# Kernel tuning notes

Hardware: AMD Instinct MI355X
Metric: run time of the kernel (lower is better)

Reference implementation:

```python
import jax, jax.numpy as jnp
import numpy as np
from jax import lax

B, N, NPOINT, NSAMPLE = 16, 8192, 1024, 32
RADIUS = 0.2
EPS = 1e-5


def setup_inputs() -> dict:
    key = jax.random.key(0)
    ks = jax.random.split(key, 6)
    return {
        "xyz": jax.random.uniform(ks[0], (B, N, 3), dtype=jnp.float32),
        "points": jax.random.normal(ks[1], (B, N, 64), dtype=jnp.float32),
        "w1": jax.random.normal(ks[2], (64, 67), dtype=jnp.float32) * 0.1,
        "b1": jnp.zeros((64,), jnp.float32),
        "g1": jnp.ones((64,), jnp.float32),
        "be1": jnp.zeros((64,), jnp.float32),
        "w2": jax.random.normal(ks[3], (64, 64), dtype=jnp.float32) * 0.1,
        "b2": jnp.zeros((64,), jnp.float32),
        "g2": jnp.ones((64,), jnp.float32),
        "be2": jnp.zeros((64,), jnp.float32),
        "w3": jax.random.normal(ks[4], (128, 64), dtype=jnp.float32) * 0.1,
        "b3": jnp.zeros((128,), jnp.float32),
        "g3": jnp.ones((128,), jnp.float32),
        "be3": jnp.zeros((128,), jnp.float32),
    }


def farthest_point_sample(xyz, npoint):
    # Sequential FPS; deterministic start at index 0 (torch uses a random start).
    b, n, _ = xyz.shape
    batch_ix = jnp.arange(b)

    def step(carry, _):
        distance, farthest = carry
        centroid = xyz[batch_ix, farthest]              # [B,3]
        dist = jnp.sum((xyz - centroid[:, None, :]) ** 2, -1)  # [B,N]
        distance = jnp.minimum(distance, dist)
        return (distance, jnp.argmax(distance, -1).astype(jnp.int32)), farthest

    init = (jnp.full((b, n), 1e10, jnp.float32), jnp.zeros((b,), jnp.int32))
    _, idxs = lax.scan(step, init, None, length=npoint)
    return idxs.T                                        # [B,npoint]


def gather_points(points, idx):
    # points [B,N,C], idx [B,...] -> [B,...,C]
    return jax.vmap(lambda p, i: p[i])(points, idx)


def query_ball_point(radius, nsample, xyz, new_xyz):
    b, n, _ = xyz.shape
    sqrd = jnp.sum((new_xyz[:, :, None, :] - xyz[:, None, :, :]) ** 2, -1)  # [B,S,N]
    gidx = jnp.where(sqrd > radius ** 2, n, jnp.arange(n, dtype=jnp.int32)[None, None, :])
    gidx = jnp.sort(gidx, axis=-1)[:, :, :nsample]       # [B,S,K]
    first = gidx[:, :, :1]
    return jnp.where(gidx == n, first, gidx)


def conv_bn_relu(x, w, b, g, be):
    # x [B,C,S,K]; 1x1 conv == channel matmul, then train-mode BN over (B,S,K).
    y = jnp.einsum("bcsk,oc->bosk", x, w) + b[None, :, None, None]
    mean = jnp.mean(y, axis=(0, 2, 3), keepdims=True)
    var = jnp.mean((y - mean) ** 2, axis=(0, 2, 3), keepdims=True)
    yhat = (y - mean) * lax.rsqrt(var + EPS)
    return jax.nn.relu(yhat * g[None, :, None, None] + be[None, :, None, None])


def reference(xyz, points, w1, b1, g1, be1, w2, b2, g2, be2, w3, b3, g3, be3):
    fps_idx = farthest_point_sample(xyz, NPOINT)          # [B,S]
    new_xyz = gather_points(xyz, fps_idx)                 # [B,S,3]
    idx = query_ball_point(RADIUS, NSAMPLE, xyz, new_xyz) # [B,S,K]
    grouped_xyz = gather_points(xyz, idx)                 # [B,S,K,3]
    grouped_xyz_norm = grouped_xyz - new_xyz[:, :, None, :]
    grouped_points = gather_points(points, idx)           # [B,S,K,64]
    new_points = jnp.concatenate([grouped_xyz_norm, grouped_points], axis=-1)
    x = jnp.transpose(new_points, (0, 3, 1, 2))           # [B,67,S,K]
    x = conv_bn_relu(x, w1, b1, g1, be1)
    x = conv_bn_relu(x, w2, b2, g2, be2)
    x = conv_bn_relu(x, w3, b3, g3, be3)
    new_points_out = jnp.max(x, axis=-1)                  # [B,128,S]
    return new_xyz, new_points_out
```

## Files before the change

kernel.cpp:

```cpp
#include <hip/hip_runtime.h>
#include <hip/hip_bf16.h>

typedef unsigned short u16;
typedef unsigned long long u64;
typedef __attribute__((ext_vector_type(8))) short short8;
typedef __attribute__((ext_vector_type(4))) float f32x4;

#define NN 8192
#define SSAMP 1024
#define KK 32
#define NT_F 524288.0f
#define EPSV 1e-5f

__device__ __forceinline__ u64 umax64(u64 a, u64 b) { return a > b ? a : b; }

template <int C>
__device__ __forceinline__ void dppstep(unsigned& hi, unsigned& lo) {
  unsigned h2 = (unsigned)__builtin_amdgcn_update_dpp(0, (int)hi, C, 0xF, 0xF, true);
  unsigned l2 = (unsigned)__builtin_amdgcn_update_dpp(0, (int)lo, C, 0xF, 0xF, true);
  u64 a = ((u64)hi << 32) | lo;
  u64 b = ((u64)h2 << 32) | l2;
  bool g = b > a;
  hi = g ? h2 : hi;
  lo = g ? l2 : lo;
}

__device__ __forceinline__ u64 wave_max_key(u64 key) {
  unsigned hi = (unsigned)(key >> 32), lo = (unsigned)key;
  dppstep<0x111>(hi, lo);
  dppstep<0x112>(hi, lo);
  dppstep<0x114>(hi, lo);
  dppstep<0x118>(hi, lo);
  dppstep<0x142>(hi, lo);
  dppstep<0x143>(hi, lo);
  return ((u64)hi << 32) | lo;
}

__device__ __forceinline__ int morton3(int ix, int iy, int iz) {
  int m = (((ix >> 0) & 1) << 2) | (((iy >> 0) & 1) << 1) | (((iz >> 0) & 1) << 0);
  m |= (((ix >> 1) & 1) << 5) | (((iy >> 1) & 1) << 4) | (((iz >> 1) & 1) << 3);
  m |= (((ix >> 2) & 1) << 8) | (((iy >> 2) & 1) << 7) | (((iz >> 2) & 1) << 6);
  return m;
}

__global__ __launch_bounds__(1024, 1) void fps_bucket_kernel(const float* __restrict__ xyz,
                                                             float* __restrict__ newxyz) {
  extern __shared__ float dynls[];
  float* sx = dynls;
  float* sy = dynls + NN;
  float* sz = dynls + 2 * NN;
  int* sI = (int*)(dynls + 3 * NN);
  __shared__ int cnt[512], off[512];
  __shared__ u64 candS[3];
  __shared__ int pos0_sh;

  const int b = blockIdx.x, t = threadIdx.x;
  const float* base = xyz + (size_t)b * NN * 3;

  float px[8], py[8], pz[8];
  int pc[8];
  if (t < 512) cnt[t] = 0;
  if (t == 0) { candS[0] = 0; candS[1] = 0; candS[2] = 0; }
  __syncthreads();
#pragma unroll
  for (int j = 0; j < 8; j++) {
    int p = j * 1024 + t;
    px[j] = base[p * 3 + 0];
    py[j] = base[p * 3 + 1];
    pz[j] = base[p * 3 + 2];
    int ix = min(7, (int)(px[j] * 8.0f));
    int iy = min(7, (int)(py[j] * 8.0f));
    int iz = min(7, (int)(pz[j] * 8.0f));
    pc[j] = morton3(ix, iy, iz);
    atomicAdd(&cnt[pc[j]], 1);
  }
  __syncthreads();
  int myc = (t < 512) ? cnt[t] : 0;
  for (int st = 1; st < 512; st <<= 1) {
    int v = 0;
    if (t < 512) { v = cnt[t]; if (t >= st) v += cnt[t - st]; }
    __syncthreads();
    if (t < 512) cnt[t] = v;
    __syncthreads();
  }
  if (t < 512) off[t] = cnt[t] - myc;
  __syncthreads();
#pragma unroll
  for (int j = 0; j < 8; j++) {
    int pos = atomicAdd(&off[pc[j]], 1);
    sx[pos] = px[j]; sy[pos] = py[j]; sz[pos] = pz[j];
    int orig = j * 1024 + t;
    sI[pos] = orig;
    if (orig == 0) pos0_sh = pos;
  }
  __syncthreads();
  float X[8], Y[8], Z[8], D[8];
  unsigned L26[8];
  float lox = 1e30f, loy = 1e30f, loz = 1e30f;
  float hix = -1e30f, hiy = -1e30f, hiz = -1e30f;
#pragma unroll
  for (int j = 0; j < 8; j++) {
    int p = t * 8 + j;
    float x = sx[p], y = sy[p], z = sz[p];
    X[j] = x; Y[j] = y; Z[j] = z; D[j] = 1e10f;
    int orig = sI[p];
    L26[j] = ((unsigned)(8191 - orig) << 13) | (unsigned)p;
    lox = fminf(lox, x); hix = fmaxf(hix, x);
    loy = fminf(loy, y); hiy = fmaxf(hiy, y);
    loz = fminf(loz, z); hiz = fmaxf(hiz, z);
  }
  int cur = pos0_sh;
  u64 ckey = 0;
  float cbd = 1e30f;
  u64 wkeyS = 0;
  int s = 0;

  for (int it = 0; it < SSAMP; it++) {
    const int sn = (s == 2) ? 0 : s + 1;
    float cx = sx[cur], cy = sy[cur], cz = sz[cur];
    if (t == 0) {
      float* o = newxyz + ((size_t)b * SSAMP + it) * 3;
      o[0] = cx; o[1] = cy; o[2] = cz;
    }
    float ddx = fmaxf(fmaxf(lox - cx, cx - hix), 0.f);
    float ddy = fmaxf(fmaxf(loy - cy, cy - hiy), 0.f);
    float ddz = fmaxf(fmaxf(loz - cz, cz - hiz), 0.f);
    float lb2 = fmaf(ddx, ddx, fmaf(ddy, ddy, ddz * ddz));
    bool upd = lb2 <= fmaf(cbd, 1.0001f, 1e-12f);
    if (__ballot(upd)) {
      if (upd) {
        u64 k = 0;
        float bd = -1.0f;
#pragma unroll
        for (int j = 0; j < 8; j++) {
          float dx = __fsub_rn(X[j], cx);
          float dy = __fsub_rn(Y[j], cy);
          float dz = __fsub_rn(Z[j], cz);
          float d = __fadd_rn(__fadd_rn(__fmul_rn(dx, dx), __fmul_rn(dy, dy)), __fmul_rn(dz, dz));
          float dm = fminf(D[j], d);
          D[j] = dm;
          bd = fmaxf(bd, dm);
          u64 kj = ((u64)__float_as_uint(dm) << 26) | (u64)L26[j];
          k = umax64(k, kj);
        }
        ckey = k;
        cbd = bd;
      }
      wkeyS = wave_max_key(ckey);
    }
    if ((t & 63) == 63) atomicMax(&candS[s], wkeyS);
    if (t == 0) candS[sn] = 0;
    __syncthreads();
    cur = (int)(candS[s] & 0x1FFFull);
    s = sn;
  }
}

__global__ __launch_bounds__(512, 1) void fps_fallback_kernel(const float* __restrict__ xyz,
                                                              float* __restrict__ newxyz) {
  const int b = blockIdx.x, t = threadIdx.x;
  const float* base = xyz + (size_t)b * NN * 3;
  __shared__ u64 cand[2][8];
  float X[16], Y[16], Z[16], D[16];
#pragma unroll
  for (int j = 0; j < 16; j++) {
    int p = j * 512 + t;
    X[j] = base[p * 3 + 0];
    Y[j] = base[p * 3 + 1];
    Z[j] = base[p * 3 + 2];
    D[j] = 1e10f;
  }
  __syncthreads();
  int cur = 0;
  const int w = t >> 6;
  for (int it = 0; it < SSAMP; it++) {
    float cx = base[cur * 3 + 0];
    float cy = base[cur * 3 + 1];
    float cz = base[cur * 3 + 2];
    if (t == 0) {
      float* o = newxyz + ((size_t)b * SSAMP + it) * 3;
      o[0] = cx; o[1] = cy; o[2] = cz;
    }
    float bestd = -1.0f;
    int bj = 0;
#pragma unroll
    for (int j = 0; j < 16; j++) {
      float dx = __fsub_rn(X[j], cx);
      float dy = __fsub_rn(Y[j], cy);
      float dz = __fsub_rn(Z[j], cz);
      float d = __fadd_rn(__fadd_rn(__fmul_rn(dx, dx), __fmul_rn(dy, dy)), __fmul_rn(dz, dz));
      float dm = fminf(D[j], d);
      D[j] = dm;
      bool g = dm > bestd;
      bestd = g ? dm : bestd;
      bj = g ? j : bj;
    }
    u64 key = ((u64)__float_as_uint(bestd) << 32) |
              (u64)(unsigned)~(unsigned)(bj * 512 + t);
    key = wave_max_key(key);
    const int s = it & 1;
    if ((t & 63) == 63) cand[s][w] = key;
    __syncthreads();
    u64 c0 = cand[s][0], c1 = cand[s][1], c2 = cand[s][2], c3 = cand[s][3];
    u64 c4 = cand[s][4], c5 = cand[s][5], c6 = cand[s][6], c7 = cand[s][7];
    u64 a0 = umax64(c0, c1), a1 = umax64(c2, c3), a2 = umax64(c4, c5), a3 = umax64(c6, c7);
    u64 best = umax64(umax64(a0, a1), umax64(a2, a3));
    cur = (int)(~(unsigned)(best & 0xFFFFFFFFull));
  }
}

__global__ __launch_bounds__(256) void ballq_kernel(const float* __restrict__ xyz,
                                                    const float* __restrict__ newxyz,
                                                    int* __restrict__ ballidx) {
  const int wid = blockIdx.x * 4 + (threadIdx.x >> 6);
  const int lane = threadIdx.x & 63;
  const int b = wid >> 10;
  const float* base = xyz + (size_t)b * NN * 3;
  const float cx = newxyz[wid * 3 + 0];
  const float cy = newxyz[wid * 3 + 1];
  const float cz = newxyz[wid * 3 + 2];
  int* op = ballidx + (size_t)wid * KK;
  int cnt = 0, first = -1;
  for (int p0 = 0; p0 < NN; p0 += 64) {
    const int p = p0 + lane;
    float dx = __fsub_rn(cx, base[p * 3 + 0]);
    float dy = __fsub_rn(cy, base[p * 3 + 1]);
    float dz = __fsub_rn(cz, base[p * 3 + 2]);
    float d = __fadd_rn(__fadd_rn(__fmul_rn(dx, dx), __fmul_rn(dy, dy)), __fmul_rn(dz, dz));
    bool hit = d <= 0.04f;
    u64 m = __ballot(hit);
    if (m) {
      if (first < 0) first = p0 + __ffsll((long long)m) - 1;
      int rank = __popcll(m & ((1ull << lane) - 1ull));
      int slot = cnt + rank;
      if (hit && slot < KK) op[slot] = p;
      cnt += __popcll(m);
      if (cnt >= KK) break;
    }
  }
  if (cnt < KK && lane >= cnt && lane < KK) op[lane] = first;
}

__device__ __forceinline__ void stage_W(const float* __restrict__ w, float* Ws, int K, int O, int t) {
  for (int i2 = t; i2 < K * O; i2 += 256) {
    int c = i2 / O, o = i2 % O;
    Ws[i2] = w[o * K + c];
  }
}

__global__ __launch_bounds__(256) void gemm1_kernel(const float* __restrict__ xyz,
                                                    const float* __restrict__ pts,
                                                    const float* __restrict__ w1,
                                                    const float* __restrict__ b1,
                                                    const float* __restrict__ newxyz,
                                                    const int* __restrict__ ballidx,
                                                    u16* __restrict__ Y1,
                                                    float* __restrict__ bkt) {
  __shared__ __align__(16) float As[67 * 64];
  __shared__ __align__(16) float Ws[67 * 64];
  __shared__ int sidx[64];
  __shared__ float snx[6];
  const int t = threadIdx.x, blk = blockIdx.x;
  const int pbase = blk * 64;
  const int g0 = pbase >> 5;
  const int b = g0 >> 10;
  if (t < 64) sidx[t] = ballidx[pbase + t];
  if (t < 6) snx[t] = newxyz[(size_t)g0 * 3 + t];
  stage_W(w1, Ws, 67, 64, t);
  __syncthreads();
  {
    int r = t >> 2, q = t & 3;
    const float4* prow = (const float4*)(pts + ((size_t)b * NN + sidx[r]) * 64);
#pragma unroll
    for (int l = 0; l < 4; l++) {
      float4 v = prow[q * 4 + l];
      int c = 3 + q * 16 + l * 4;
      As[(c + 0) * 64 + r] = v.x;
      As[(c + 1) * 64 + r] = v.y;
      As[(c + 2) * 64 + r] = v.z;
      As[(c + 3) * 64 + r] = v.w;
    }
  }
  if (t < 64) {
    const float* xp = xyz + ((size_t)b * NN + sidx[t]) * 3;
    int g = t >> 5;
    As[0 * 64 + t] = xp[0] - snx[g * 3 + 0];
    As[1 * 64 + t] = xp[1] - snx[g * 3 + 1];
    As[2 * 64 + t] = xp[2] - snx[g * 3 + 2];
  }
  __syncthreads();
  const int i = t & 15, j = t >> 4;
  float acc[4][4];
#pragma unroll
  for (int a = 0; a < 4; a++)
#pragma unroll
    for (int c2 = 0; c2 < 4; c2++) acc[a][c2] = 0.f;
#pragma unroll 4
  for (int c = 0; c < 67; c++) {
    float4 a4 = *(const float4*)&As[c * 64 + i * 4];
    float4 w4 = *(const float4*)&Ws[c * 64 + j * 4];
    float av[4] = {a4.x, a4.y, a4.z, a4.w};
    float wv[4] = {w4.x, w4.y, w4.z, w4.w};
#pragma unroll
    for (int ii = 0; ii < 4; ii++)
#pragma unroll
      for (int jj = 0; jj < 4; jj++) acc[ii][jj] = fmaf(av[ii], wv[jj], acc[ii][jj]);
  }
  float bl[4];
#pragma unroll
  for (int jj = 0; jj < 4; jj++) bl[jj] = b1[j * 4 + jj];
#pragma unroll
  for (int ii = 0; ii < 4; ii++) {
    union { ushort4 u4; __hip_bfloat16 h[4]; } pk;
#pragma unroll
    for (int jj = 0; jj < 4; jj++) {
      float y = acc[ii][jj] + bl[jj];
      acc[ii][jj] = y;
      pk.h[jj] = __float2bfloat16(y);
    }
    *(ushort4*)&Y1[((size_t)(pbase + i * 4 + ii)) * 64 + j * 4] = pk.u4;
  }
  float sums[4], sqs[4];
#pragma unroll
  for (int jj = 0; jj < 4; jj++) {
    float s = 0.f, q2 = 0.f;
#pragma unroll
    for (int ii = 0; ii < 4; ii++) { float v = acc[ii][jj]; s += v; q2 += v * v; }
    sums[jj] = s; sqs[jj] = q2;
  }
#pragma unroll
  for (int off = 1; off < 16; off <<= 1) {
#pragma unroll
    for (int jj = 0; jj < 4; jj++) {
      sums[jj] += __shfl_xor(sums[jj], off);
      sqs[jj] += __shfl_xor(sqs[jj], off);
    }
  }
  if ((t & 15) == 0) {
    float* bb = bkt + (size_t)(blk & 63) * 512;
#pragma unroll
    for (int jj = 0; jj < 4; jj++) {
      atomicAdd(&bb[j * 4 + jj], sums[jj]);
      atomicAdd(&bb[64 + j * 4 + jj], sqs[jj]);
    }
  }
}

__global__ __launch_bounds__(256) void collapse_kernel(const float* __restrict__ bkt,
                                                       float* __restrict__ dst) {
  int e = blockIdx.x * 256 + threadIdx.x;
  float s = 0.f;
#pragma unroll 8
  for (int u = 0; u < 64; u++) s += bkt[u * 512 + e];
  dst[e] = s;
}

__device__ __forceinline__ short8 bn_pack8(const u16 h[8], const float* sS, const float* sT, int c0) {
  short8 r;
#pragma unroll
  for (int x = 0; x < 8; x++) {
    float f = __bfloat162float(*(const __hip_bfloat16*)&h[x]);
    f = fmaxf(fmaf(f, sS[c0 + x], sT[c0 + x]), 0.f);
    __hip_bfloat16 hb = __float2bfloat16(f);
    r[x] = *(const short*)&hb;
  }
  return r;
}

__device__ __forceinline__ short8 w_pack8(const float v[8]) {
  short8 r;
#pragma unroll
  for (int x = 0; x < 8; x++) {
    __hip_bfloat16 hb = __float2bfloat16(v[x]);
    r[x] = *(const short*)&hb;
  }
  return r;
}

__global__ __launch_bounds__(256) void gemm2_mfma_kernel(u16* __restrict__ Y,
                                                         const float* __restrict__ w2,
                                                         const float* __restrict__ b2,
                                                         const float* __restrict__ g1,
                                                         const float* __restrict__ be1,
                                                         const float* __restrict__ statsC,
                                                         float* __restrict__ bkt) {
  __shared__ __align__(16) short Af[8 * 64 * 8];
  __shared__ __align__(16) short Bf[8 * 64 * 8];
  __shared__ __align__(16) u16 Cs[64 * 72];
  __shared__ float sS[64], sT[64];
  __shared__ float sSum[64], sSq[64];
  const int t = threadIdx.x, blk = blockIdx.x;
  const int pbase = blk * 64;
  if (t < 64) {
    float mean = statsC[t] * (1.0f / NT_F);
    float var = statsC[64 + t] * (1.0f / NT_F) - mean * mean;
    float s = g1[t] * rsqrtf(var + EPSV);
    sS[t] = s;
    sT[t] = be1[t] - mean * s;
  }
  __syncthreads();
  {
    int r = t >> 2, q = t & 3;
    const uint4* yrow = (const uint4*)(Y + (size_t)(pbase + r) * 64);
    union { uint4 u; u16 h[8]; } v0, v1;
    v0.u = yrow[q * 2]; v1.u = yrow[q * 2 + 1];
    int c0 = q * 16;
    int kt = c0 >> 5, mt = r >> 4;
    int qp0 = (c0 >> 3) & 3, qp1 = ((c0 + 8) >> 3) & 3;
    *(short8*)&Af[(((mt << 1) | kt) * 64 + qp0 * 16 + (r & 15)) * 8] = bn_pack8(v0.h, sS, sT, c0);
    *(short8*)&Af[(((mt << 1) | kt) * 64 + qp1 * 16 + (r & 15)) * 8] = bn_pack8(v1.h, sS, sT, c0 + 8);
  }
  {
    int o = t >> 2, q = t & 3;
    const float* wrow = w2 + o * 64 + q * 16;
    float f0[8], f1[8];
#pragma unroll
    for (int x = 0; x < 8; x++) { f0[x] = wrow[x]; f1[x] = wrow[8 + x]; }
    int c0 = q * 16;
    int kt = c0 >> 5, nt = o >> 4;
    int qp0 = (c0 >> 3) & 3, qp1 = ((c0 + 8) >> 3) & 3;
    *(short8*)&Bf[(((nt << 1) | kt) * 64 + qp0 * 16 + (o & 15)) * 8] = w_pack8(f0);
    *(short8*)&Bf[(((nt << 1) | kt) * 64 + qp1 * 16 + (o & 15)) * 8] = w_pack8(f1);
  }
  __syncthreads();
  const int w = t >> 6, L = t & 63, q = L >> 4;
  const int nt = w;
  short8 b0 = *(const short8*)&Bf[((nt * 2 + 0) * 64 + L) * 8];
  short8 b1 = *(const short8*)&Bf[((nt * 2 + 1) * 64 + L) * 8];
  const int o = nt * 16 + (L & 15);
  const float bl = b2[o];
  f32x4 acc[4];
#pragma unroll
  for (int mt = 0; mt < 4; mt++) {
    acc[mt] = (f32x4){0.f, 0.f, 0.f, 0.f};
    short8 a0 = *(const short8*)&Af[((mt * 2 + 0) * 64 + L) * 8];
    short8 a1 = *(const short8*)&Af[((mt * 2 + 1) * 64 + L) * 8];
    acc[mt] = __builtin_amdgcn_mfma_f32_16x16x32_bf16(a0, b0, acc[mt], 0, 0, 0);
    acc[mt] = __builtin_amdgcn_mfma_f32_16x16x32_bf16(a1, b1, acc[mt], 0, 0, 0);
  }
  float s = 0.f, q2 = 0.f;
#pragma unroll
  for (int mt = 0; mt < 4; mt++) {
#pragma unroll
    for (int r = 0; r < 4; r++) {
      float y = acc[mt][r] + bl;
      s += y; q2 += y * y;
      __hip_bfloat16 hb = __float2bfloat16(y);
      Cs[(mt * 16 + q * 4 + r) * 72 + o] = *(const u16*)&hb;
    }
  }
  s += __shfl_xor(s, 16); s += __shfl_xor(s, 32);
  q2 += __shfl_xor(q2, 16); q2 += __shfl_xor(q2, 32);
  if (L < 16) { sSum[o] = s; sSq[o] = q2; }
  __syncthreads();
  {
    int r = t >> 2, qq = t & 3;
    uint4 c0 = *(const uint4*)&Cs[r * 72 + qq * 16];
    uint4 c1 = *(const uint4*)&Cs[r * 72 + qq * 16 + 8];
    uint4* yrow = (uint4*)(Y + (size_t)(pbase + r) * 64);
    yrow[qq * 2] = c0; yrow[qq * 2 + 1] = c1;
  }
  float* bb = bkt + (size_t)(blk & 63) * 512;
  if (t < 64) atomicAdd(&bb[128 + t], sSum[t]);
  else if (t < 128) atomicAdd(&bb[192 + (t - 64)], sSq[t - 64]);
}

__global__ __launch_bounds__(256) void conv3max_mfma_kernel(const u16* __restrict__ Y,
                                                            const float* __restrict__ w3,
                                                            const float* __restrict__ b3,
                                                            const float* __restrict__ g2,
                                                            const float* __restrict__ be2,
                                                            const float* __restrict__ statsC,
                                                            float* __restrict__ bkt,
                                                            float* __restrict__ gmax,
                                                            float* __restrict__ gmin) {
  __shared__ __align__(16) short Af[8 * 64 * 8];
  __shared__ __align__(16) short Bf[16 * 64 * 8];
  __shared__ float sS[64], sT[64];
  __shared__ float sSum[128], sSq[128];
  const int t = threadIdx.x, blk = blockIdx.x;
  const int pbase = blk * 64;
  if (t < 64) {
    float mean = statsC[128 + t] * (1.0f / NT_F);
    float var = statsC[192 + t] * (1.0f / NT_F) - mean * mean;
    float s = g2[t] * rsqrtf(var + EPSV);
    sS[t] = s;
    sT[t] = be2[t] - mean * s;
  }
  __syncthreads();
  {
    int r = t >> 2, q = t & 3;
    const uint4* yrow = (const uint4*)(Y + (size_t)(pbase + r) * 64);
    union { uint4 u; u16 h[8]; } v0, v1;
    v0.u = yrow[q * 2]; v1.u = yrow[q * 2 + 1];
    int c0 = q * 16;
    int kt = c0 >> 5, mt = r >> 4;
    int qp0 = (c0 >> 3) & 3, qp1 = ((c0 + 8) >> 3) & 3;
    *(short8*)&Af[(((mt << 1) | kt) * 64 + qp0 * 16 + (r & 15)) * 8] = bn_pack8(v0.h, sS, sT, c0);
    *(short8*)&Af[(((mt << 1) | kt) * 64 + qp1 * 16 + (r & 15)) * 8] = bn_pack8(v1.h, sS, sT, c0 + 8);
  }
  {
    int o = t >> 1, h = t & 1;
    const float* wrow = w3 + o * 64 + h * 32;
    int nt = o >> 4;
#pragma unroll
    for (int g = 0; g < 4; g++) {
      float f[8];
#pragma unroll
      for (int x = 0; x < 8; x++) f[x] = wrow[g * 8 + x];
      *(short8*)&Bf[(((nt << 1) | h) * 64 + g * 16 + (o & 15)) * 8] = w_pack8(f);
    }
  }
  __syncthreads();
  const int w = t >> 6, L = t & 63, q = L >> 4;
  f32x4 acc[2][4];
#pragma unroll
  for (int n = 0; n < 2; n++)
#pragma unroll
    for (int mt = 0; mt < 4; mt++) acc[n][mt] = (f32x4){0.f, 0.f, 0.f, 0.f};
  short8 bfr[2][2];
#pragma unroll
  for (int n = 0; n < 2; n++) {
    int nt = 2 * w + n;
    bfr[n][0] = *(const short8*)&Bf[((nt * 2 + 0) * 64 + L) * 8];
    bfr[n][1] = *(const short8*)&Bf[((nt * 2 + 1) * 64 + L) * 8];
  }
#pragma unroll
  for (int mt = 0; mt < 4; mt++) {
    short8 a0 = *(const short8*)&Af[((mt * 2 + 0) * 64 + L) * 8];
    short8 a1 = *(const short8*)&Af[((mt * 2 + 1) * 64 + L) * 8];
#pragma unroll
    for (int n = 0; n < 2; n++) {
      acc[n][mt] = __builtin_amdgcn_mfma_f32_16x16x32_bf16(a0, bfr[n][0], acc[n][mt], 0, 0, 0);
      acc[n][mt] = __builtin_amdgcn_mfma_f32_16x16x32_bf16(a1, bfr[n][1], acc[n][mt], 0, 0, 0);
    }
  }
#pragma unroll
  for (int n = 0; n < 2; n++) {
    int o = (2 * w + n) * 16 + (L & 15);
    float bl = b3[o];
    float s = 0.f, q2 = 0.f;
    float gmx[2] = {-1e30f, -1e30f}, gmn[2] = {1e30f, 1e30f};
#pragma unroll
    for (int mt = 0; mt < 4; mt++) {
      int g = mt >> 1;
#pragma unroll
      for (int r = 0; r < 4; r++) {
        float y = acc[n][mt][r] + bl;
        s += y; q2 += y * y;
        gmx[g] = fmaxf(gmx[g], y);
        gmn[g] = fminf(gmn[g], y);
      }
    }
    s += __shfl_xor(s, 16); s += __shfl_xor(s, 32);
    q2 += __shfl_xor(q2, 16); q2 += __shfl_xor(q2, 32);
#pragma unroll
    for (int g = 0; g < 2; g++) {
      gmx[g] = fmaxf(gmx[g], __shfl_xor(gmx[g], 16));
      gmx[g] = fmaxf(gmx[g], __shfl_xor(gmx[g], 32));
      gmn[g] = fminf(gmn[g], __shfl_xor(gmn[g], 16));
      gmn[g] = fminf(gmn[g], __shfl_xor(gmn[g], 32));
    }
    if (L < 16) {
      sSum[o] = s; sSq[o] = q2;
#pragma unroll
      for (int g = 0; g < 2; g++) {
        gmax[(size_t)(blk * 2 + g) * 128 + o] = gmx[g];
        gmin[(size_t)(blk * 2 + g) * 128 + o] = gmn[g];
      }
    }
  }
  __syncthreads();
  float* bb = bkt + (size_t)(blk & 63) * 512;
  if (t < 128) atomicAdd(&bb[256 + t], sSum[t]);
  else atomicAdd(&bb[384 + (t - 128)], sSq[t - 128]);
}

__global__ __launch_bounds__(256) void finalize_kernel(const float* __restrict__ gmax,
                                                       const float* __restrict__ gmin,
                                                       const float* __restrict__ statsC,
                                                       const float* __restrict__ g3,
                                                       const float* __restrict__ be3,
                                                       float* __restrict__ outf) {
  __shared__ float smax[64 * 65], smin[64 * 65];
  __shared__ float ssc[64], ssh[64];
  const int t = threadIdx.x, blk = blockIdx.x;
  const int b = blk >> 5, st = (blk >> 1) & 15, oh = blk & 1;
  const int o0 = oh * 64, g0 = b * 1024 + st * 64;
  if (t < 64) {
    int o = o0 + t;
    float mean = statsC[256 + o] * (1.0f / NT_F);
    float var = statsC[384 + o] * (1.0f / NT_F) - mean * mean;
    float sc = g3[o] * rsqrtf(var + EPSV);
    ssc[t] = sc;
    ssh[t] = be3[o] - mean * sc;
  }
  const int col = t & 63, rw = t >> 6;
#pragma unroll
  for (int k = 0; k < 16; k++) {
    int r = k * 4 + rw;
    smax[r * 65 + col] = gmax[(size_t)(g0 + r) * 128 + o0 + col];
    smin[r * 65 + col] = gmin[(size_t)(g0 + r) * 128 + o0 + col];
  }
  __syncthreads();
#pragma unroll
  for (int k = 0; k < 16; k++) {
    int o = k * 4 + rw;
    float sc = ssc[o], sh = ssh[o];
    float v = sc > 0.f ? smax[col * 65 + o] : smin[col * 65 + o];
    outf[((size_t)(b * 128 + o0 + o)) * 1024 + st * 64 + col] = fmaxf(fmaf(v, sc, sh), 0.f);
  }
}

extern "C" void kernel_launch(void* const* d_in, const int* in_sizes, int n_in,
                              void* d_out, int out_size, void* d_ws, size_t ws_size,
                              hipStream_t stream) {
  const float* xyz = (const float*)d_in[0];
  const float* pts = (const float*)d_in[1];
  const float* w1 = (const float*)d_in[2];
  const float* b1 = (const float*)d_in[3];
  const float* g1 = (const float*)d_in[4];
  const float* be1 = (const float*)d_in[5];
  const float* w2 = (const float*)d_in[6];
  const float* b2 = (const float*)d_in[7];
  const float* g2 = (const float*)d_in[8];
  const float* be2 = (const float*)d_in[9];
  const float* w3 = (const float*)d_in[10];
  const float* b3 = (const float*)d_in[11];
  const float* g3 = (const float*)d_in[12];
  const float* be3 = (const float*)d_in[13];

  float* out = (float*)d_out;
  float* newxyz = out;
  float* outfeat = out + 49152;

  char* ws = (char*)d_ws;
  int* ballidx = (int*)ws;
  float* bkt = (float*)(ws + (2 << 20));
  float* statsC = (float*)(ws + (2 << 20) + 131072);
  float* gmax = (float*)(ws + (4 << 20));
  float* gmin = (float*)(ws + (12 << 20));
  u16* Y = (u16*)(ws + (20 << 20));

  hipMemsetAsync(bkt, 0, 64 * 512 * sizeof(float), stream);

  bool use_bucket = false;
  {
    hipError_t e = hipFuncSetAttribute((const void*)fps_bucket_kernel,
                                       hipFuncAttributeMaxDynamicSharedMemorySize, 131072);
    if (e == hipSuccess) {
      int nb = 0;
      hipError_t e2 = hipOccupancyMaxActiveBlocksPerMultiprocessor(
          &nb, (const void*)fps_bucket_kernel, 1024, 131072);
      use_bucket = (e2 == hipSuccess && nb >= 1);
    }
  }
  if (use_bucket)
    fps_bucket_kernel<<<16, 1024, 131072, stream>>>(xyz, newxyz);
  else
    fps_fallback_kernel<<<16, 512, 0, stream>>>(xyz, newxyz);

  ballq_kernel<<<4096, 256, 0, stream>>>(xyz, newxyz, ballidx);
  gemm1_kernel<<<8192, 256, 0, stream>>>(xyz, pts, w1, b1, newxyz, ballidx, Y, bkt);
  collapse_kernel<<<2, 256, 0, stream>>>(bkt, statsC);
  gemm2_mfma_kernel<<<8192, 256, 0, stream>>>(Y, w2, b2, g1, be1, statsC, bkt);
  collapse_kernel<<<2, 256, 0, stream>>>(bkt, statsC);
  conv3max_mfma_kernel<<<8192, 256, 0, stream>>>(Y, w3, b3, g2, be2, statsC, bkt, gmax, gmin);
  collapse_kernel<<<2, 256, 0, stream>>>(bkt, statsC);
  finalize_kernel<<<512, 256, 0, stream>>>(gmax, gmin, statsC, g3, be3, outfeat);
}
```

Before: 1.324 ms.

## Port first conv to bf16 MFMA and pack FPS shared data as float4

Replaces the scalar fp32 FMA gemm1 kernel with a bf16 MFMA version. Gathered point features, xyz offsets and weights are packed into MFMA fragment layouts in shared memory, with K padded from 67 to 96. Per-channel sums are reduced in shared memory before fewer global atomics. The FPS kernel now stores points as float4 (xyz plus original index) so the centroid read is one LDS load, and splits the per-iteration atomicMax across four slots to reduce contention. This adds bf16 rounding to the first layer's inputs and weights, which may shift BN statistics slightly.

Result: faster. 1.269 ms (-4.1%).

```diff
diff --git a/kernel.cpp b/kernel.cpp
--- a/kernel.cpp
+++ b/kernel.cpp
@@ -45,13 +45,9 @@
 
 __global__ __launch_bounds__(1024, 1) void fps_bucket_kernel(const float* __restrict__ xyz,
                                                              float* __restrict__ newxyz) {
-  extern __shared__ float dynls[];
-  float* sx = dynls;
-  float* sy = dynls + NN;
-  float* sz = dynls + 2 * NN;
-  int* sI = (int*)(dynls + 3 * NN);
+  extern __shared__ float4 sp4[];
   __shared__ int cnt[512], off[512];
-  __shared__ u64 candS[3];
+  __shared__ u64 candS[3][4];
   __shared__ int pos0_sh;
 
   const int b = blockIdx.x, t = threadIdx.x;
@@ -60,7 +56,7 @@
   float px[8], py[8], pz[8];
   int pc[8];
   if (t < 512) cnt[t] = 0;
-  if (t == 0) { candS[0] = 0; candS[1] = 0; candS[2] = 0; }
+  if (t < 12) candS[t >> 2][t & 3] = 0;
   __syncthreads();
 #pragma unroll
   for (int j = 0; j < 8; j++) {
@@ -88,9 +84,8 @@
 #pragma unroll
   for (int j = 0; j < 8; j++) {
     int pos = atomicAdd(&off[pc[j]], 1);
-    sx[pos] = px[j]; sy[pos] = py[j]; sz[pos] = pz[j];
     int orig = j * 1024 + t;
-    sI[pos] = orig;
+    sp4[pos] = make_float4(px[j], py[j], pz[j], __int_as_float(orig));
     if (orig == 0) pos0_sh = pos;
   }
   __syncthreads();
@@ -101,15 +96,16 @@
 #pragma unroll
   for (int j = 0; j < 8; j++) {
     int p = t * 8 + j;
-    float x = sx[p], y = sy[p], z = sz[p];
-    X[j] = x; Y[j] = y; Z[j] = z; D[j] = 1e10f;
-    int orig = sI[p];
+    float4 v = sp4[p];
+    X[j] = v.x; Y[j] = v.y; Z[j] = v.z; D[j] = 1e10f;
+    int orig = __float_as_int(v.w);
     L26[j] = ((unsigned)(8191 - orig) << 13) | (unsigned)p;
-    lox = fminf(lox, x); hix = fmaxf(hix, x);
-    loy = fminf(loy, y); hiy = fmaxf(hiy, y);
-    loz = fminf(loz, z); hiz = fmaxf(hiz, z);
+    lox = fminf(lox, v.x); hix = fmaxf(hix, v.x);
+    loy = fminf(loy, v.y); hiy = fmaxf(hiy, v.y);
+    loz = fminf(loz, v.z); hiz = fmaxf(hiz, v.z);
   }
   int cur = pos0_sh;
+  const int w = t >> 6, sl = w & 3;
   u64 ckey = 0;
   float cbd = 1e30f;
   u64 wkeyS = 0;
@@ -117,7 +113,8 @@
 
   for (int it = 0; it < SSAMP; it++) {
     const int sn = (s == 2) ? 0 : s + 1;
-    float cx = sx[cur], cy = sy[cur], cz = sz[cur];
+    float4 c4 = sp4[cur];
+    float cx = c4.x, cy = c4.y, cz = c4.z;
     if (t == 0) {
       float* o = newxyz + ((size_t)b * SSAMP + it) * 3;
       o[0] = cx; o[1] = cy; o[2] = cz;
@@ -148,10 +145,12 @@
       }
       wkeyS = wave_max_key(ckey);
     }
-    if ((t & 63) == 63) atomicMax(&candS[s], wkeyS);
-    if (t == 0) candS[sn] = 0;
+    if ((t & 63) == 63) atomicMax(&candS[s][sl], wkeyS);
+    if (t < 4) candS[sn][t] = 0;
     __syncthreads();
-    cur = (int)(candS[s] & 0x1FFFull);
+    u64 m0 = umax64(candS[s][0], candS[s][1]);
+    u64 m1 = umax64(candS[s][2], candS[s][3]);
+    cur = (int)(umax64(m0, m1) & 0x1FFFull);
     s = sn;
   }
 }
@@ -241,111 +240,6 @@
   if (cnt < KK && lane >= cnt && lane < KK) op[lane] = first;
 }
 
-__device__ __forceinline__ void stage_W(const float* __restrict__ w, float* Ws, int K, int O, int t) {
-  for (int i2 = t; i2 < K * O; i2 += 256) {
-    int c = i2 / O, o = i2 % O;
-    Ws[i2] = w[o * K + c];
-  }
-}
-
-__global__ __launch_bounds__(256) void gemm1_kernel(const float* __restrict__ xyz,
-                                                    const float* __restrict__ pts,
-                                                    const float* __restrict__ w1,
-                                                    const float* __restrict__ b1,
-                                                    const float* __restrict__ newxyz,
-                                                    const int* __restrict__ ballidx,
-                                                    u16* __restrict__ Y1,
-                                                    float* __restrict__ bkt) {
-  __shared__ __align__(16) float As[67 * 64];
-  __shared__ __align__(16) float Ws[67 * 64];
-  __shared__ int sidx[64];
-  __shared__ float snx[6];
-  const int t = threadIdx.x, blk = blockIdx.x;
-  const int pbase = blk * 64;
-  const int g0 = pbase >> 5;
-  const int b = g0 >> 10;
-  if (t < 64) sidx[t] = ballidx[pbase + t];
-  if (t < 6) snx[t] = newxyz[(size_t)g0 * 3 + t];
-  stage_W(w1, Ws, 67, 64, t);
-  __syncthreads();
-  {
-    int r = t >> 2, q = t & 3;
-    const float4* prow = (const float4*)(pts + ((size_t)b * NN + sidx[r]) * 64);
-#pragma unroll
-    for (int l = 0; l < 4; l++) {
-      float4 v = prow[q * 4 + l];
-      int c = 3 + q * 16 + l * 4;
-      As[(c + 0) * 64 + r] = v.x;
-      As[(c + 1) * 64 + r] = v.y;
-      As[(c + 2) * 64 + r] = v.z;
-      As[(c + 3) * 64 + r] = v.w;
-    }
-  }
-  if (t < 64) {
-    const float* xp = xyz + ((size_t)b * NN + sidx[t]) * 3;
-    int g = t >> 5;
-    As[0 * 64 + t] = xp[0] - snx[g * 3 + 0];
-    As[1 * 64 + t] = xp[1] - snx[g * 3 + 1];
-    As[2 * 64 + t] = xp[2] - snx[g * 3 + 2];
-  }
-  __syncthreads();
-  const int i = t & 15, j = t >> 4;
-  float acc[4][4];
-#pragma unroll
-  for (int a = 0; a < 4; a++)
-#pragma unroll
-    for (int c2 = 0; c2 < 4; c2++) acc[a][c2] = 0.f;
-#pragma unroll 4
-  for (int c = 0; c < 67; c++) {
-    float4 a4 = *(const float4*)&As[c * 64 + i * 4];
-    float4 w4 = *(const float4*)&Ws[c * 64 + j * 4];
-    float av[4] = {a4.x, a4.y, a4.z, a4.w};
-    float wv[4] = {w4.x, w4.y, w4.z, w4.w};
-#pragma unroll
-    for (int ii = 0; ii < 4; ii++)
-#pragma unroll
-      for (int jj = 0; jj < 4; jj++) acc[ii][jj] = fmaf(av[ii], wv[jj], acc[ii][jj]);
-  }
-  float bl[4];
-#pragma unroll
-  for (int jj = 0; jj < 4; jj++) bl[jj] = b1[j * 4 + jj];
-#pragma unroll
-  for (int ii = 0; ii < 4; ii++) {
-    union { ushort4 u4; __hip_bfloat16 h[4]; } pk;
-#pragma unroll
-    for (int jj = 0; jj < 4; jj++) {
-      float y = acc[ii][jj] + bl[jj];
-      acc[ii][jj] = y;
-      pk.h[jj] = __float2bfloat16(y);
-    }
-    *(ushort4*)&Y1[((size_t)(pbase + i * 4 + ii)) * 64 + j * 4] = pk.u4;
-  }
-  float sums[4], sqs[4];
-#pragma unroll
-  for (int jj = 0; jj < 4; jj++) {
-    float s = 0.f, q2 = 0.f;
-#pragma unroll
-    for (int ii = 0; ii < 4; ii++) { float v = acc[ii][jj]; s += v; q2 += v * v; }
-    sums[jj] = s; sqs[jj] = q2;
-  }
-#pragma unroll
-  for (int off = 1; off < 16; off <<= 1) {
-#pragma unroll
-    for (int jj = 0; jj < 4; jj++) {
-      sums[jj] += __shfl_xor(sums[jj], off);
-      sqs[jj] += __shfl_xor(sqs[jj], off);
-    }
-  }
-  if ((t & 15) == 0) {
-    float* bb = bkt + (size_t)(blk & 63) * 512;
-#pragma unroll
-    for (int jj = 0; jj < 4; jj++) {
-      atomicAdd(&bb[j * 4 + jj], sums[jj]);
-      atomicAdd(&bb[64 + j * 4 + jj], sqs[jj]);
-    }
-  }
-}
-
 __global__ __launch_bounds__(256) void collapse_kernel(const float* __restrict__ bkt,
                                                        float* __restrict__ dst) {
   int e = blockIdx.x * 256 + threadIdx.x;
@@ -375,6 +269,125 @@
     r[x] = *(const short*)&hb;
   }
   return r;
+}
+
+__global__ __launch_bounds__(256) void gemm1_mfma_kernel(const float* __restrict__ xyz,
+                                                         const float* __restrict__ pts,
+                                                         const float* __restrict__ w1,
+                                                         const float* __restrict__ b1,
+                                                         const float* __restrict__ newxyz,
+                                                         const int* __restrict__ ballidx,
+                                                         u16* __restrict__ Y,
+                                                         float* __restrict__ bkt) {
+  __shared__ __align__(16) short Af[12 * 64 * 8];
+  __shared__ __align__(16) short Bf[12 * 64 * 8];
+  __shared__ __align__(16) u16 Cs[64 * 72];
+  __shared__ int sidx[64];
+  __shared__ float snx[6];
+  __shared__ float sSum[64], sSq[64];
+  const int t = threadIdx.x, blk = blockIdx.x;
+  const int pbase = blk * 64;
+  const int g0 = pbase >> 5;
+  const int b = g0 >> 10;
+  if (t < 64) sidx[t] = ballidx[pbase + t];
+  if (t < 6) snx[t] = newxyz[(size_t)g0 * 3 + t];
+  __syncthreads();
+  {
+    int r = t >> 2, q = t & 3;
+    const float4* prow = (const float4*)(pts + ((size_t)b * NN + sidx[r]) * 64);
+    float4 v0 = prow[q * 4 + 0], v1 = prow[q * 4 + 1];
+    float4 v2 = prow[q * 4 + 2], v3 = prow[q * 4 + 3];
+    float f0[8] = {v0.x, v0.y, v0.z, v0.w, v1.x, v1.y, v1.z, v1.w};
+    float f1[8] = {v2.x, v2.y, v2.z, v2.w, v3.x, v3.y, v3.z, v3.w};
+    int kt = q >> 1, mt = r >> 4, m = r & 15;
+    int qp0 = (2 * q) & 3, qp1 = (2 * q + 1) & 3;
+    *(short8*)&Af[((mt * 3 + kt) * 64 + qp0 * 16 + m) * 8] = w_pack8(f0);
+    *(short8*)&Af[((mt * 3 + kt) * 64 + qp1 * 16 + m) * 8] = w_pack8(f1);
+  }
+  {
+    int o = t >> 2, q = t & 3;
+    const float* wr = w1 + o * 67 + 3 + q * 16;
+    float f0[8], f1[8];
+#pragma unroll
+    for (int x = 0; x < 8; x++) { f0[x] = wr[x]; f1[x] = wr[8 + x]; }
+    int kt = q >> 1, nt = o >> 4, n = o & 15;
+    int qp0 = (2 * q) & 3, qp1 = (2 * q + 1) & 3;
+    *(short8*)&Bf[((nt * 3 + kt) * 64 + qp0 * 16 + n) * 8] = w_pack8(f0);
+    *(short8*)&Bf[((nt * 3 + kt) * 64 + qp1 * 16 + n) * 8] = w_pack8(f1);
+  }
+  if (t < 64) {
+    const float* xp = xyz + ((size_t)b * NN + sidx[t]) * 3;
+    int g = t >> 5, mt = t >> 4, m = t & 15;
+    float xn = xp[0] - snx[g * 3 + 0];
+    float yn = xp[1] - snx[g * 3 + 1];
+    float zn = xp[2] - snx[g * 3 + 2];
+    short8 s0 = {0, 0, 0, 0, 0, 0, 0, 0};
+    short8 z8 = {0, 0, 0, 0, 0, 0, 0, 0};
+    __hip_bfloat16 hb;
+    hb = __float2bfloat16(xn); s0[0] = *(const short*)&hb;
+    hb = __float2bfloat16(yn); s0[1] = *(const short*)&hb;
+    hb = __float2bfloat16(zn); s0[2] = *(const short*)&hb;
+    *(short8*)&Af[((mt * 3 + 2) * 64 + 0 * 16 + m) * 8] = s0;
+    *(short8*)&Af[((mt * 3 + 2) * 64 + 1 * 16 + m) * 8] = z8;
+    *(short8*)&Af[((mt * 3 + 2) * 64 + 2 * 16 + m) * 8] = z8;
+    *(short8*)&Af[((mt * 3 + 2) * 64 + 3 * 16 + m) * 8] = z8;
+  } else if (t < 128) {
+    int o = t - 64, nt = o >> 4, n = o & 15;
+    short8 s0 = {0, 0, 0, 0, 0, 0, 0, 0};
+    short8 z8 = {0, 0, 0, 0, 0, 0, 0, 0};
+    __hip_bfloat16 hb;
+    hb = __float2bfloat16(w1[o * 67 + 0]); s0[0] = *(const short*)&hb;
+    hb = __float2bfloat16(w1[o * 67 + 1]); s0[1] = *(const short*)&hb;
+    hb = __float2bfloat16(w1[o * 67 + 2]); s0[2] = *(const short*)&hb;
+    *(short8*)&Bf[((nt * 3 + 2) * 64 + 0 * 16 + n) * 8] = s0;
+    *(short8*)&Bf[((nt * 3 + 2) * 64 + 1 * 16 + n) * 8] = z8;
+    *(short8*)&Bf[((nt * 3 + 2) * 64 + 2 * 16 + n) * 8] = z8;
+    *(short8*)&Bf[((nt * 3 + 2) * 64 + 3 * 16 + n) * 8] = z8;
+  }
+  __syncthreads();
+  const int w = t >> 6, L = t & 63, q = L >> 4;
+  const int nt = w;
+  short8 b0 = *(const short8*)&Bf[((nt * 3 + 0) * 64 + L) * 8];
+  short8 b1v = *(const short8*)&Bf[((nt * 3 + 1) * 64 + L) * 8];
+  short8 b2v = *(const short8*)&Bf[((nt * 3 + 2) * 64 + L) * 8];
+  const int o = nt * 16 + (L & 15);
+  const float bl = b1[o];
+  f32x4 acc[4];
+#pragma unroll
+  for (int mt = 0; mt < 4; mt++) {
+    acc[mt] = (f32x4){0.f, 0.f, 0.f, 0.f};
+    short8 a0 = *(const short8*)&Af[((mt * 3 + 0) * 64 + L) * 8];
+    short8 a1 = *(const short8*)&Af[((mt * 3 + 1) * 64 + L) * 8];
+    short8 a2 = *(const short8*)&Af[((mt * 3 + 2) * 64 + L) * 8];
+    acc[mt] = __builtin_amdgcn_mfma_f32_16x16x32_bf16(a0, b0, acc[mt], 0, 0, 0);
+    acc[mt] = __builtin_amdgcn_mfma_f32_16x16x32_bf16(a1, b1v, acc[mt], 0, 0, 0);
+    acc[mt] = __builtin_amdgcn_mfma_f32_16x16x32_bf16(a2, b2v, acc[mt], 0, 0, 0);
+  }
+  float s = 0.f, q2 = 0.f;
+#pragma unroll
+  for (int mt = 0; mt < 4; mt++) {
+#pragma unroll
+    for (int r = 0; r < 4; r++) {
+      float y = acc[mt][r] + bl;
+      s += y; q2 += y * y;
+      __hip_bfloat16 hb = __float2bfloat16(y);
+      Cs[(mt * 16 + q * 4 + r) * 72 + o] = *(const u16*)&hb;
+    }
+  }
+  s += __shfl_xor(s, 16); s += __shfl_xor(s, 32);
+  q2 += __shfl_xor(q2, 16); q2 += __shfl_xor(q2, 32);
+  if (L < 16) { sSum[o] = s; sSq[o] = q2; }
+  __syncthreads();
+  {
+    int r = t >> 2, qq = t & 3;
+    uint4 c0 = *(const uint4*)&Cs[r * 72 + qq * 16];
+    uint4 c1 = *(const uint4*)&Cs[r * 72 + qq * 16 + 8];
+    uint4* yrow = (uint4*)(Y + (size_t)(pbase + r) * 64);
+    yrow[qq * 2] = c0; yrow[qq * 2 + 1] = c1;
+  }
+  float* bb = bkt + (size_t)(blk & 63) * 512;
+  if (t < 64) atomicAdd(&bb[t], sSum[t]);
+  else if (t < 128) atomicAdd(&bb[64 + (t - 64)], sSq[t - 64]);
 }
 
 __global__ __launch_bounds__(256) void gemm2_mfma_kernel(u16* __restrict__ Y,
@@ -661,7 +674,7 @@
     fps_fallback_kernel<<<16, 512, 0, stream>>>(xyz, newxyz);
 
   ballq_kernel<<<4096, 256, 0, stream>>>(xyz, newxyz, ballidx);
-  gemm1_kernel<<<8192, 256, 0, stream>>>(xyz, pts, w1, b1, newxyz, ballidx, Y, bkt);
+  gemm1_mfma_kernel<<<8192, 256, 0, stream>>>(xyz, pts, w1, b1, newxyz, ballidx, Y, bkt);
   collapse_kernel<<<2, 256, 0, stream>>>(bkt, statsC);
   gemm2_mfma_kernel<<<8192, 256, 0, stream>>>(Y, w2, b2, g1, be1, statsC, bkt);
   collapse_kernel<<<2, 256, 0, stream>>>(bkt, statsC);
```
